# Kernel optimization log

Hardware: AMD Instinct MI355X
Metric: run time of the kernel (lower is better)

## Reference

```python
import jax, jax.numpy as jnp
import numpy as np

B, S, D, H = 4, 2048, 1024, 16
HD = D // H


def setup_inputs() -> dict:
    key = jax.random.key(0)
    ks = jax.random.split(key, 12)
    scale = 1.0 / np.sqrt(D)
    inp = {
        "query": jax.random.normal(ks[0], (B, S, D), jnp.float32),
        "key": jax.random.normal(ks[1], (B, S, D), jnp.float32),
        "value": jax.random.normal(ks[2], (B, S, D), jnp.float32),
        "mask": jax.random.randint(ks[3], (B, 1, S, S), 0, 2).astype(jnp.float32),
        "Wq": jax.random.normal(ks[4], (D, D), jnp.float32) * scale,
        "bq": jnp.zeros((D,), jnp.float32),
        "Wk": jax.random.normal(ks[5], (D, D), jnp.float32) * scale,
        "bk": jnp.zeros((D,), jnp.float32),
        "Wv": jax.random.normal(ks[6], (D, D), jnp.float32) * scale,
        "bv": jnp.zeros((D,), jnp.float32),
        "Wo": jax.random.normal(ks[7], (D, D), jnp.float32) * scale,
        "bo": jnp.zeros((D,), jnp.float32),
    }
    return inp


def reference(query, key, value, mask, Wq, bq, Wk, bk, Wv, bv, Wo, bo):
    # projections, then split heads: [B, S, D] -> [B, H, S, HD]
    def split_heads(x):
        return x.reshape(B, S, H, HD).transpose(0, 2, 1, 3)

    q = split_heads(query @ Wq + bq)
    k = split_heads(key @ Wk + bk)
    v = split_heads(value @ Wv + bv)

    # scores [B, H, Sq, Sk]
    logits = jnp.einsum("bhqd,bhkd->bhqk", q, k) / jnp.sqrt(jnp.float32(HD))
    logits = logits + mask * (-1e9)
    attn = jax.nn.softmax(logits, axis=-1)
    out = jnp.einsum("bhqk,bhkd->bhqd", attn, v)  # [B, H, Sq, HD]
    out = out.transpose(0, 2, 1, 3).reshape(B, S, D)
    return out @ Wo + bo
```

## Files before the change

kernel.cpp:

```cpp
#include <hip/hip_runtime.h>

#define DI __device__ __forceinline__

typedef __attribute__((ext_vector_type(8))) short short8v;
typedef __attribute__((ext_vector_type(4))) float f32x4;

static constexpr int B_ = 4, S_ = 2048, D_ = 1024, H_ = 16, HD_ = 64;
static constexpr int M_ = B_ * S_;

DI unsigned short f2bf(float f) {
  unsigned u = __builtin_bit_cast(unsigned, f);
  u = (u + 0x7fffu + ((u >> 16) & 1u)) >> 16;
  return (unsigned short)u;
}

DI void async_copy16(const void* g, void* l) {
  __builtin_amdgcn_global_load_lds((const __attribute__((address_space(1))) void*)g,
                                   (__attribute__((address_space(3))) void*)l, 16, 0, 0);
}

__global__ __launch_bounds__(256) void cast_bf16_kernel(const float* __restrict__ in,
                                                        unsigned short* __restrict__ out,
                                                        int n4) {
  int i = blockIdx.x * blockDim.x + threadIdx.x;
  int stride = gridDim.x * blockDim.x;
  for (; i < n4; i += stride) {
    float4 v = reinterpret_cast<const float4*>(in)[i];
    ushort4 o;
    o.x = f2bf(v.x); o.y = f2bf(v.y); o.z = f2bf(v.z); o.w = f2bf(v.w);
    reinterpret_cast<ushort4*>(out)[i] = o;
  }
}

__global__ __launch_bounds__(256) void transpose_cast_kernel(const float* __restrict__ W,
                                                             unsigned short* __restrict__ Wt,
                                                             int n) {
  __shared__ float t[32][33];
  int bx = blockIdx.x * 32, by = blockIdx.y * 32;
  int x = threadIdx.x, y0 = threadIdx.y;
#pragma unroll
  for (int yy = 0; yy < 32; yy += 8)
    t[y0 + yy][x] = W[(long)(by + y0 + yy) * n + bx + x];
  __syncthreads();
#pragma unroll
  for (int yy = 0; yy < 32; yy += 8)
    Wt[(long)(bx + y0 + yy) * n + by + x] = f2bf(t[x][y0 + yy]);
}

__global__ __launch_bounds__(256) void pack_mask_kernel(const float* __restrict__ mask,
                                                        unsigned long long* __restrict__ bits,
                                                        int nwords) {
  int lane = threadIdx.x & 63;
  int wpb = blockDim.x >> 6;
  int w = blockIdx.x * wpb + (threadIdx.x >> 6);
  int stride = gridDim.x * wpb;
  for (; w < nwords; w += stride) {
    float v = mask[(long)w * 64 + lane];
    unsigned long long b = __ballot(v > 0.5f);
    if (lane == 0) bits[w] = b;
  }
}

template <int MODE>
__global__ __launch_bounds__(256) void gemm_bt_kernel(const unsigned short* __restrict__ A,
                                                      const unsigned short* __restrict__ Bt,
                                                      const float* __restrict__ bias,
                                                      void* __restrict__ out,
                                                      int Mdim, int Ndim, int Kdim, float scale) {
  __shared__ unsigned short As[128 * 32];
  __shared__ unsigned short Bs[128 * 32];
  const int tid = threadIdx.x;
  const int lane = tid & 63;
  const int w = tid >> 6;
  const int g = lane >> 4;
  const int l15 = lane & 15;
  const int bm = blockIdx.x * 128;
  const int bn = blockIdx.y * 128;
  const int wr = w >> 1, wc = w & 1;

  f32x4 zero = {0.f, 0.f, 0.f, 0.f};
  f32x4 acc[4][4];
#pragma unroll
  for (int i = 0; i < 4; ++i)
#pragma unroll
    for (int j = 0; j < 4; ++j) acc[i][j] = zero;

  const int srow = lane >> 2;
  const int scol = (lane & 3) * 8;

  for (int k0 = 0; k0 < Kdim; k0 += 32) {
#pragma unroll
    for (int i = 0; i < 2; ++i) {
      int q = w * 2 + i;
      int row = q * 16 + srow;
      async_copy16(&A[(long)(bm + row) * Kdim + k0 + scol], &As[q * 512]);
      async_copy16(&Bt[(long)(bn + row) * Kdim + k0 + scol], &Bs[q * 512]);
    }
    __syncthreads();
    short8v a[4], b[4];
#pragma unroll
    for (int i = 0; i < 4; ++i)
      a[i] = *reinterpret_cast<const short8v*>(&As[(wr * 64 + i * 16 + l15) * 32 + g * 8]);
#pragma unroll
    for (int j = 0; j < 4; ++j)
      b[j] = *reinterpret_cast<const short8v*>(&Bs[(wc * 64 + j * 16 + l15) * 32 + g * 8]);
#pragma unroll
    for (int i = 0; i < 4; ++i)
#pragma unroll
      for (int j = 0; j < 4; ++j)
        acc[i][j] = __builtin_amdgcn_mfma_f32_16x16x32_bf16(a[i], b[j], acc[i][j], 0, 0, 0);
    __syncthreads();
  }

#pragma unroll
  for (int jj = 0; jj < 4; ++jj) {
    int n = bn + wc * 64 + jj * 16 + l15;
    float bs = bias[n];
#pragma unroll
    for (int i = 0; i < 4; ++i) {
      int m0 = bm + wr * 64 + i * 16 + g * 4;
      if (MODE == 0) {
        unsigned short* o = (unsigned short*)out;
#pragma unroll
        for (int r = 0; r < 4; ++r)
          o[(long)(m0 + r) * Ndim + n] = f2bf((acc[i][jj][r] + bs) * scale);
      } else if (MODE == 1) {
        int b2 = m0 >> 11, s0 = m0 & 2047;
        int h2 = n >> 6, d2 = n & 63;
        unsigned short* o = (unsigned short*)out;
        ushort4 v;
        v.x = f2bf(acc[i][jj][0] + bs);
        v.y = f2bf(acc[i][jj][1] + bs);
        v.z = f2bf(acc[i][jj][2] + bs);
        v.w = f2bf(acc[i][jj][3] + bs);
        *reinterpret_cast<ushort4*>(&o[((long)((b2 * 16 + h2) * 64 + d2) << 11) + s0]) = v;
      } else {
        float* o = (float*)out;
#pragma unroll
        for (int r = 0; r < 4; ++r)
          o[(long)(m0 + r) * Ndim + n] = acc[i][jj][r] + bs;
      }
    }
  }
}

__global__ __launch_bounds__(256, 3) void attn_kernel(const unsigned short* __restrict__ Q,
                                                      const unsigned short* __restrict__ Kb,
                                                      const unsigned short* __restrict__ Vt,
                                                      const unsigned long long* __restrict__ mbits,
                                                      unsigned short* __restrict__ attn) {
  __shared__ unsigned short Ks[64 * 64];
  __shared__ unsigned short Vs[64 * 64];
  __shared__ unsigned short plds[4][2][16][72];
  const int lane = threadIdx.x & 63;
  const int w = threadIdx.x >> 6;
  const int g = lane >> 4;
  const int l15 = lane & 15;
  const int qt = blockIdx.x;
  const int bh = blockIdx.y;
  const int b = bh >> 4, h = bh & 15;
  const int q0 = qt * 128 + w * 32 + l15;

  const unsigned short* qp = Q + ((long)b * S_ + q0) * D_ + h * HD_ + g * 8;
  short8v qfr[2][2];
  qfr[0][0] = *reinterpret_cast<const short8v*>(qp);
  qfr[0][1] = *reinterpret_cast<const short8v*>(qp + 32);
  qfr[1][0] = *reinterpret_cast<const short8v*>(qp + 16 * D_);
  qfr[1][1] = *reinterpret_cast<const short8v*>(qp + 16 * D_ + 32);

  const int srow = lane >> 3;
  const int schunk = ((lane & 7) ^ (lane >> 3)) * 8;
  const unsigned short* kstage = Kb + (long)b * S_ * D_ + h * HD_;
  const unsigned short* vstage = Vt + (long)bh * HD_ * S_;

  f32x4 zero = {0.f, 0.f, 0.f, 0.f};
  f32x4 oacc[2][4];
#pragma unroll
  for (int qf = 0; qf < 2; ++qf)
#pragma unroll
    for (int d = 0; d < 4; ++d) oacc[qf][d] = zero;
  float m_run[2] = {-1e30f, -1e30f}, l_run[2] = {0.f, 0.f};

  const unsigned long long* mrow[2];
  mrow[0] = mbits + ((long)b * S_ + q0) * (S_ / 64);
  mrow[1] = mrow[0] + 16 * (S_ / 64);
  const int swz = l15 & 7;

  for (int kt = 0; kt < S_; kt += 64) {
#pragma unroll
    for (int i = 0; i < 2; ++i) {
      int blk8 = w * 2 + i;
      async_copy16(&kstage[(long)(kt + blk8 * 8 + srow) * D_ + schunk], &Ks[blk8 * 512]);
      async_copy16(&vstage[(long)(blk8 * 8 + srow) * S_ + kt + schunk], &Vs[blk8 * 512]);
    }
    __syncthreads();

    f32x4 lt[2][4];
#pragma unroll
    for (int g2 = 0; g2 < 4; ++g2) {
      const unsigned short* kr = &Ks[(g2 * 16 + l15) * 64];
      short8v kf0 = *reinterpret_cast<const short8v*>(&kr[(g ^ swz) * 8]);
      short8v kf1 = *reinterpret_cast<const short8v*>(&kr[((g + 4) ^ swz) * 8]);
#pragma unroll
      for (int qf = 0; qf < 2; ++qf) {
        f32x4 c = zero;
        c = __builtin_amdgcn_mfma_f32_16x16x32_bf16(kf0, qfr[qf][0], c, 0, 0, 0);
        c = __builtin_amdgcn_mfma_f32_16x16x32_bf16(kf1, qfr[qf][1], c, 0, 0, 0);
        lt[qf][g2] = c;
      }
    }

    short8v pf[2][2];
#pragma unroll
    for (int qf = 0; qf < 2; ++qf) {
      unsigned long long mw = mrow[qf][kt >> 6];
      float tmax = -1e30f;
#pragma unroll
      for (int g2 = 0; g2 < 4; ++g2)
#pragma unroll
        for (int r = 0; r < 4; ++r) {
          int krel = g2 * 16 + g * 4 + r;
          float v = ((mw >> krel) & 1ull) ? -1e30f : lt[qf][g2][r];
          lt[qf][g2][r] = v;
          tmax = fmaxf(tmax, v);
        }
      tmax = fmaxf(tmax, __shfl_xor(tmax, 16));
      tmax = fmaxf(tmax, __shfl_xor(tmax, 32));
      float m_new = fmaxf(m_run[qf], tmax);
      float alpha = __expf(m_run[qf] - m_new);
      float tsum = 0.f;
#pragma unroll
      for (int g2 = 0; g2 < 4; ++g2) {
        float p0 = __expf(lt[qf][g2][0] - m_new);
        float p1 = __expf(lt[qf][g2][1] - m_new);
        float p2 = __expf(lt[qf][g2][2] - m_new);
        float p3 = __expf(lt[qf][g2][3] - m_new);
        tsum += p0 + p1 + p2 + p3;
        ushort4 pk;
        pk.x = f2bf(p0); pk.y = f2bf(p1); pk.z = f2bf(p2); pk.w = f2bf(p3);
        *reinterpret_cast<ushort4*>(&plds[w][qf][l15][g2 * 16 + g * 4]) = pk;
      }
      tsum += __shfl_xor(tsum, 16);
      tsum += __shfl_xor(tsum, 32);
      l_run[qf] = l_run[qf] * alpha + tsum;
      m_run[qf] = m_new;
#pragma unroll
      for (int d = 0; d < 4; ++d) oacc[qf][d] *= alpha;
      pf[qf][0] = *reinterpret_cast<const short8v*>(&plds[w][qf][l15][g * 8]);
      pf[qf][1] = *reinterpret_cast<const short8v*>(&plds[w][qf][l15][32 + g * 8]);
    }

#pragma unroll
    for (int d0 = 0; d0 < 4; ++d0) {
      const unsigned short* vr = &Vs[(d0 * 16 + l15) * 64];
      short8v vf0 = *reinterpret_cast<const short8v*>(&vr[(g ^ swz) * 8]);
      short8v vf1 = *reinterpret_cast<const short8v*>(&vr[((g + 4) ^ swz) * 8]);
#pragma unroll
      for (int qf = 0; qf < 2; ++qf) {
        oacc[qf][d0] = __builtin_amdgcn_mfma_f32_16x16x32_bf16(vf0, pf[qf][0], oacc[qf][d0], 0, 0, 0);
        oacc[qf][d0] = __builtin_amdgcn_mfma_f32_16x16x32_bf16(vf1, pf[qf][1], oacc[qf][d0], 0, 0, 0);
      }
    }
    __syncthreads();
  }

#pragma unroll
  for (int qf = 0; qf < 2; ++qf) {
    float inv = 1.f / l_run[qf];
    int q = q0 + qf * 16;
#pragma unroll
    for (int d0 = 0; d0 < 4; ++d0) {
      ushort4 o;
      o.x = f2bf(oacc[qf][d0][0] * inv);
      o.y = f2bf(oacc[qf][d0][1] * inv);
      o.z = f2bf(oacc[qf][d0][2] * inv);
      o.w = f2bf(oacc[qf][d0][3] * inv);
      *reinterpret_cast<ushort4*>(&attn[((long)b * S_ + q) * D_ + h * HD_ + d0 * 16 + g * 4]) = o;
    }
  }
}

extern "C" void kernel_launch(void* const* d_in, const int* in_sizes, int n_in,
                              void* d_out, int out_size, void* d_ws, size_t ws_size,
                              hipStream_t stream) {
  const float* query = (const float*)d_in[0];
  const float* key   = (const float*)d_in[1];
  const float* value = (const float*)d_in[2];
  const float* mask  = (const float*)d_in[3];
  const float* Wq = (const float*)d_in[4];
  const float* bq = (const float*)d_in[5];
  const float* Wk = (const float*)d_in[6];
  const float* bk = (const float*)d_in[7];
  const float* Wv = (const float*)d_in[8];
  const float* bv = (const float*)d_in[9];
  const float* Wo = (const float*)d_in[10];
  const float* bo = (const float*)d_in[11];

  char* ws = (char*)d_ws;
  unsigned short* XQ  = (unsigned short*)(ws);
  unsigned short* XK  = (unsigned short*)(ws + (16ull << 20));
  unsigned short* XV  = (unsigned short*)(ws + (32ull << 20));
  unsigned short* WQT = (unsigned short*)(ws + (48ull << 20));
  unsigned short* WKT = (unsigned short*)(ws + (50ull << 20));
  unsigned short* WVT = (unsigned short*)(ws + (52ull << 20));
  unsigned short* WOT = (unsigned short*)(ws + (54ull << 20));
  unsigned short* QB  = (unsigned short*)(ws + (56ull << 20));
  unsigned short* KB  = (unsigned short*)(ws + (72ull << 20));
  unsigned short* VT  = (unsigned short*)(ws + (88ull << 20));
  unsigned long long* MBITS = (unsigned long long*)(ws + (16ull << 20));
  unsigned short* ATTN = XQ;

  const int n4 = M_ * D_ / 4;
  cast_bf16_kernel<<<2048, 256, 0, stream>>>(query, XQ, n4);
  cast_bf16_kernel<<<2048, 256, 0, stream>>>(key,   XK, n4);
  cast_bf16_kernel<<<2048, 256, 0, stream>>>(value, XV, n4);

  dim3 tg(D_ / 32, D_ / 32), tb(32, 8);
  transpose_cast_kernel<<<tg, tb, 0, stream>>>(Wq, WQT, D_);
  transpose_cast_kernel<<<tg, tb, 0, stream>>>(Wk, WKT, D_);
  transpose_cast_kernel<<<tg, tb, 0, stream>>>(Wv, WVT, D_);
  transpose_cast_kernel<<<tg, tb, 0, stream>>>(Wo, WOT, D_);

  dim3 gg(M_ / 128, D_ / 128);
  gemm_bt_kernel<0><<<gg, 256, 0, stream>>>(XQ, WQT, bq, QB, M_, D_, D_, 0.125f);
  gemm_bt_kernel<0><<<gg, 256, 0, stream>>>(XK, WKT, bk, KB, M_, D_, D_, 1.f);
  gemm_bt_kernel<1><<<gg, 256, 0, stream>>>(XV, WVT, bv, VT, M_, D_, D_, 1.f);

  pack_mask_kernel<<<2048, 256, 0, stream>>>(mask, MBITS, B_ * S_ * S_ / 64);

  dim3 ag(S_ / 128, B_ * H_);
  attn_kernel<<<ag, 256, 0, stream>>>(QB, KB, VT, MBITS, ATTN);

  gemm_bt_kernel<2><<<gg, 256, 0, stream>>>(ATTN, WOT, bo, d_out, M_, D_, D_, 1.f);
}
```

Measured before the change: 338.7 us.

## Keep softmax probabilities in registers by permuting V layout and mask bits

The attention kernel no longer round-trips the bf16 probabilities through shared memory. The V-transpose store permutes sequence positions so the MFMA output fragment layout can serve directly as the B operand, and P is packed with v_cvt_pk_bf16_f32. The softmax switches to exp2 with log2(e) folded into the Q scale, and the mask bitmask is re-laid out so per-tile words are indexed by key tile then query, for coalesced loads. This relies on the permutation exactly matching the fragment layout, a correctness risk in exchange for less LDS traffic and fewer instructions.

Result: faster. 311.2 us (-8.1%).

```diff
diff --git a/kernel.cpp b/kernel.cpp
--- a/kernel.cpp
+++ b/kernel.cpp
@@ -12,6 +12,12 @@
   unsigned u = __builtin_bit_cast(unsigned, f);
   u = (u + 0x7fffu + ((u >> 16) & 1u)) >> 16;
   return (unsigned short)u;
+}
+
+DI unsigned cvt_pk_bf16(float lo, float hi) {
+  unsigned r;
+  asm("v_cvt_pk_bf16_f32 %0, %1, %2" : "=v"(r) : "v"(lo), "v"(hi));
+  return r;
 }
 
 DI void async_copy16(const void* g, void* l) {
@@ -57,7 +63,10 @@
   for (; w < nwords; w += stride) {
     float v = mask[(long)w * 64 + lane];
     unsigned long long b = __ballot(v > 0.5f);
-    if (lane == 0) bits[w] = b;
+    if (lane == 0) {
+      int bb = w >> 16, q = (w >> 5) & 2047, kt64 = w & 31;
+      bits[((long)bb << 16) | (kt64 << 11) | q] = b;
+    }
   }
 }
 
@@ -126,6 +135,7 @@
           o[(long)(m0 + r) * Ndim + n] = f2bf((acc[i][jj][r] + bs) * scale);
       } else if (MODE == 1) {
         int b2 = m0 >> 11, s0 = m0 & 2047;
+        int s0p = (s0 & ~31) | (((s0 >> 2) & 3) << 3) | (((s0 >> 4) & 1) << 2);
         int h2 = n >> 6, d2 = n & 63;
         unsigned short* o = (unsigned short*)out;
         ushort4 v;
@@ -133,7 +143,7 @@
         v.y = f2bf(acc[i][jj][1] + bs);
         v.z = f2bf(acc[i][jj][2] + bs);
         v.w = f2bf(acc[i][jj][3] + bs);
-        *reinterpret_cast<ushort4*>(&o[((long)((b2 * 16 + h2) * 64 + d2) << 11) + s0]) = v;
+        *reinterpret_cast<ushort4*>(&o[((long)((b2 * 16 + h2) * 64 + d2) << 11) + s0p]) = v;
       } else {
         float* o = (float*)out;
 #pragma unroll
@@ -151,7 +161,6 @@
                                                       unsigned short* __restrict__ attn) {
   __shared__ unsigned short Ks[64 * 64];
   __shared__ unsigned short Vs[64 * 64];
-  __shared__ unsigned short plds[4][2][16][72];
   const int lane = threadIdx.x & 63;
   const int w = threadIdx.x >> 6;
   const int g = lane >> 4;
@@ -181,12 +190,12 @@
     for (int d = 0; d < 4; ++d) oacc[qf][d] = zero;
   float m_run[2] = {-1e30f, -1e30f}, l_run[2] = {0.f, 0.f};
 
-  const unsigned long long* mrow[2];
-  mrow[0] = mbits + ((long)b * S_ + q0) * (S_ / 64);
-  mrow[1] = mrow[0] + 16 * (S_ / 64);
+  const unsigned long long* mbase = mbits + ((long)b << 16);
   const int swz = l15 & 7;
 
   for (int kt = 0; kt < S_; kt += 64) {
+    unsigned long long mw0 = mbase[((kt >> 6) << 11) + q0];
+    unsigned long long mw1 = mbase[((kt >> 6) << 11) + q0 + 16];
 #pragma unroll
     for (int i = 0; i < 2; ++i) {
       int blk8 = w * 2 + i;
@@ -210,10 +219,10 @@
       }
     }
 
-    short8v pf[2][2];
+    short8v pfr[2][2];
 #pragma unroll
     for (int qf = 0; qf < 2; ++qf) {
-      unsigned long long mw = mrow[qf][kt >> 6];
+      unsigned long long mw = qf ? mw1 : mw0;
       float tmax = -1e30f;
 #pragma unroll
       for (int g2 = 0; g2 < 4; ++g2)
@@ -227,38 +236,42 @@
       tmax = fmaxf(tmax, __shfl_xor(tmax, 16));
       tmax = fmaxf(tmax, __shfl_xor(tmax, 32));
       float m_new = fmaxf(m_run[qf], tmax);
-      float alpha = __expf(m_run[qf] - m_new);
+      float alpha = __builtin_amdgcn_exp2f(m_run[qf] - m_new);
+      float p[4][4];
       float tsum = 0.f;
 #pragma unroll
-      for (int g2 = 0; g2 < 4; ++g2) {
-        float p0 = __expf(lt[qf][g2][0] - m_new);
-        float p1 = __expf(lt[qf][g2][1] - m_new);
-        float p2 = __expf(lt[qf][g2][2] - m_new);
-        float p3 = __expf(lt[qf][g2][3] - m_new);
-        tsum += p0 + p1 + p2 + p3;
-        ushort4 pk;
-        pk.x = f2bf(p0); pk.y = f2bf(p1); pk.z = f2bf(p2); pk.w = f2bf(p3);
-        *reinterpret_cast<ushort4*>(&plds[w][qf][l15][g2 * 16 + g * 4]) = pk;
-      }
+      for (int g2 = 0; g2 < 4; ++g2)
+#pragma unroll
+        for (int r = 0; r < 4; ++r) {
+          p[g2][r] = __builtin_amdgcn_exp2f(lt[qf][g2][r] - m_new);
+          tsum += p[g2][r];
+        }
       tsum += __shfl_xor(tsum, 16);
       tsum += __shfl_xor(tsum, 32);
       l_run[qf] = l_run[qf] * alpha + tsum;
       m_run[qf] = m_new;
 #pragma unroll
       for (int d = 0; d < 4; ++d) oacc[qf][d] *= alpha;
-      pf[qf][0] = *reinterpret_cast<const short8v*>(&plds[w][qf][l15][g * 8]);
-      pf[qf][1] = *reinterpret_cast<const short8v*>(&plds[w][qf][l15][32 + g * 8]);
+#pragma unroll
+      for (int s = 0; s < 2; ++s) {
+        union { unsigned u[4]; short8v v; } pu;
+        pu.u[0] = cvt_pk_bf16(p[2 * s][0], p[2 * s][1]);
+        pu.u[1] = cvt_pk_bf16(p[2 * s][2], p[2 * s][3]);
+        pu.u[2] = cvt_pk_bf16(p[2 * s + 1][0], p[2 * s + 1][1]);
+        pu.u[3] = cvt_pk_bf16(p[2 * s + 1][2], p[2 * s + 1][3]);
+        pfr[qf][s] = pu.v;
+      }
     }
 
 #pragma unroll
     for (int d0 = 0; d0 < 4; ++d0) {
       const unsigned short* vr = &Vs[(d0 * 16 + l15) * 64];
-      short8v vf0 = *reinterpret_cast<const short8v*>(&vr[(g ^ swz) * 8]);
-      short8v vf1 = *reinterpret_cast<const short8v*>(&vr[((g + 4) ^ swz) * 8]);
-#pragma unroll
-      for (int qf = 0; qf < 2; ++qf) {
-        oacc[qf][d0] = __builtin_amdgcn_mfma_f32_16x16x32_bf16(vf0, pf[qf][0], oacc[qf][d0], 0, 0, 0);
-        oacc[qf][d0] = __builtin_amdgcn_mfma_f32_16x16x32_bf16(vf1, pf[qf][1], oacc[qf][d0], 0, 0, 0);
+#pragma unroll
+      for (int s = 0; s < 2; ++s) {
+        short8v vf = *reinterpret_cast<const short8v*>(&vr[((s * 4 + g) ^ swz) * 8]);
+#pragma unroll
+        for (int qf = 0; qf < 2; ++qf)
+          oacc[qf][d0] = __builtin_amdgcn_mfma_f32_16x16x32_bf16(vf, pfr[qf][s], oacc[qf][d0], 0, 0, 0);
       }
     }
     __syncthreads();
@@ -322,7 +335,7 @@
   transpose_cast_kernel<<<tg, tb, 0, stream>>>(Wo, WOT, D_);
 
   dim3 gg(M_ / 128, D_ / 128);
-  gemm_bt_kernel<0><<<gg, 256, 0, stream>>>(XQ, WQT, bq, QB, M_, D_, D_, 0.125f);
+  gemm_bt_kernel<0><<<gg, 256, 0, stream>>>(XQ, WQT, bq, QB, M_, D_, D_, 0.18033688011112042f);
   gemm_bt_kernel<0><<<gg, 256, 0, stream>>>(XK, WKT, bk, KB, M_, D_, D_, 1.f);
   gemm_bt_kernel<1><<<gg, 256, 0, stream>>>(XV, WVT, bv, VT, M_, D_, D_, 1.f);
 
```
